# Kernel tuning notes

Hardware: AMD Instinct MI355X
Metric: run time of the kernel (lower is better)

Reference implementation:

```python
import jax, jax.numpy as jnp
import numpy as np

B, S, HID, H, RELC = 2, 1024, 1024, 16, 64
D = HID // H          # head dim = 64
R = 2 * RELC + 1      # 129 relative-position buckets
NEG_INF = -10000.0
LN_EPS = 1e-12


def setup_inputs() -> dict:
    key = jax.random.key(0)
    ks = jax.random.split(key, 16)
    s = 0.02
    return {
        "query": jax.random.normal(ks[0], (B, S, HID), jnp.float32),
        "key": jax.random.normal(ks[1], (B, S, HID), jnp.float32),
        "value": jax.random.normal(ks[2], (B, S, HID), jnp.float32),
        "mask_k": jnp.ones((B, S), jnp.float32),
        "mask_qk": jnp.ones((B, S, S), jnp.float32),
        "rposi": jax.random.randint(ks[3], (B, S, S), 0, R, jnp.int32),
        "Wq": jax.random.normal(ks[4], (HID, HID), jnp.float32) * s,
        "bq": jnp.zeros((HID,), jnp.float32),
        "Wk": jax.random.normal(ks[5], (HID, HID), jnp.float32) * s,
        "bk": jnp.zeros((HID,), jnp.float32),
        "Wv": jax.random.normal(ks[6], (HID, HID), jnp.float32) * s,
        "bv": jnp.zeros((HID,), jnp.float32),
        "Wd": jax.random.normal(ks[7], (HID, HID), jnp.float32) * s,
        "bd": jnp.zeros((HID,), jnp.float32),
        "ln_g": jnp.ones((HID,), jnp.float32),
        "ln_b": jnp.zeros((HID,), jnp.float32),
        "edge_atts": jax.random.normal(ks[8], (R, D), jnp.float32) * s,
        "edge_values": jax.random.normal(ks[9], (R, D), jnp.float32) * s,
    }


def _heads(x):  # [B,S,HID] -> [B,H,S,D]
    return x.reshape(B, -1, H, D).transpose(0, 2, 1, 3)


def reference(query, key, value, mask_k, mask_qk, rposi,
              Wq, bq, Wk, bk, Wv, bv, Wd, bd, ln_g, ln_b,
              edge_atts, edge_values):
    q = _heads(query @ Wq + bq)   # [B,H,Q,D]
    k = _heads(key @ Wk + bk)     # [B,H,K,D]
    v = _heads(value @ Wv + bv)   # [B,H,K,D]

    rp = jnp.clip(rposi, -RELC, RELC) + RELC          # [B,Q,K] in [0,2*RELC]

    scores = jnp.einsum('bhqd,bhkd->bhqk', q, k)      # [B,H,Q,K]
    # relative-position attention bias: q . edge_atts[rp]
    q2 = jnp.einsum('bhqd,rd->bhqr', q, edge_atts)    # [B,H,Q,R]
    rscore = jnp.take_along_axis(
        q2, jnp.broadcast_to(rp[:, None], (B, H, S, S)), axis=-1)
    scores = (scores + rscore) / jnp.sqrt(jnp.float32(D))

    att_mask = mask_k[:, None, :] * mask_qk           # [B,Q,K]
    scores = scores + (1.0 - att_mask)[:, None] * NEG_INF
    probs = jax.nn.softmax(scores, axis=-1)           # [B,H,Q,K]

    ctx = jnp.einsum('bhqk,bhkd->bhqd', probs, v)     # [B,H,Q,D]
    rval = edge_values[rp]                            # [B,Q,K,D]
    ctx = ctx + jnp.einsum('bhqk,bqkd->bhqd', probs, rval)

    ctx = ctx.transpose(0, 2, 1, 3).reshape(B, S, HID)
    h = ctx @ Wd + bd
    x = h + query
    mu = jnp.mean(x, axis=-1, keepdims=True)
    var = jnp.mean(jnp.square(x - mu), axis=-1, keepdims=True)
    return (x - mu) * jax.lax.rsqrt(var + LN_EPS) * ln_g + ln_b
```

## Files before the change

kernel.cpp:

```cpp
#include <hip/hip_runtime.h>
#include <hip/hip_bf16.h>
#include <stdint.h>

#define B_    2
#define S_    1024
#define HID_  1024
#define H_    16
#define D_    64
#define R_    129
#define RST_  132
#define NTOK_ 2048

typedef __attribute__((ext_vector_type(8))) short bf16x8;
typedef __attribute__((ext_vector_type(4))) float f32x4;

__device__ __forceinline__ float bf2f(unsigned short s) {
  union { float f; unsigned int u; } v; v.u = ((unsigned int)s) << 16; return v.f;
}
__device__ __forceinline__ unsigned short f2bf(float f) {
  union { float f; unsigned int u; } v; v.f = f;
  return (unsigned short)((v.u + 0x7fff + ((v.u >> 16) & 1)) >> 16);
}

__global__ __launch_bounds__(256) void wt4_kernel(const float* __restrict__ Wq,
                                                  const float* __restrict__ Wk,
                                                  const float* __restrict__ Wv,
                                                  const float* __restrict__ Wd,
                                                  unsigned short* __restrict__ WqT,
                                                  unsigned short* __restrict__ WkT,
                                                  unsigned short* __restrict__ WvT,
                                                  unsigned short* __restrict__ WdT) {
  const float* W; unsigned short* Wt;
  switch (blockIdx.z) {
    case 0: W = Wq; Wt = WqT; break;
    case 1: W = Wk; Wt = WkT; break;
    case 2: W = Wv; Wt = WvT; break;
    default: W = Wd; Wt = WdT; break;
  }
  __shared__ float tile[32][33];
  const int n0 = blockIdx.x * 32, k0 = blockIdx.y * 32;
  const int tx = threadIdx.x, ty = threadIdx.y;
  #pragma unroll
  for (int i = 0; i < 32; i += 8)
    tile[ty + i][tx] = W[(size_t)(k0 + ty + i) * HID_ + n0 + tx];
  __syncthreads();
  #pragma unroll
  for (int i = 0; i < 32; i += 8)
    Wt[(size_t)(n0 + ty + i) * HID_ + k0 + tx] = f2bf(tile[tx][ty + i]);
}

__global__ __launch_bounds__(256) void evt_kernel(const float* __restrict__ EV,
                                                  unsigned short* __restrict__ EVt) {
  const int idx = blockIdx.x * 256 + threadIdx.x;
  if (idx < 64 * 160) {
    const int d = idx / 160, r = idx % 160;
    EVt[idx] = f2bf(r < R_ ? EV[(size_t)r * D_ + d] : 0.f);
  }
}

__global__ __launch_bounds__(256) void rpm_kernel(const int* __restrict__ rposi,
                                                  const float* __restrict__ mask_k,
                                                  const float* __restrict__ mask_qk,
                                                  unsigned int* __restrict__ rpm) {
  const size_t base = ((size_t)blockIdx.x * 256 + threadIdx.x) * 4;
  const int b = (int)(base >> 20);
  const int k = (int)(base & (S_ - 1));
  const int4  rp4 = *(const int4*)(rposi + base);
  const float4 mq = *(const float4*)(mask_qk + base);
  const float4 mk = *(const float4*)(mask_k + (size_t)b * S_ + k);
  unsigned int o[4];
  const int rr[4] = {rp4.x, rp4.y, rp4.z, rp4.w};
  const float mm[4] = {mk.x * mq.x, mk.y * mq.y, mk.z * mq.z, mk.w * mq.w};
  #pragma unroll
  for (int u = 0; u < 4; u++) {
    const int rp = min(max(rr[u], -64), 64) + 64;
    const float bias = (1.f - mm[u]) * (-10000.0f);
    o[u] = ((unsigned int)f2bf(bias) << 16) | (unsigned int)rp;
  }
  *(uint4*)(rpm + base) = *(uint4*)o;
}

__global__ __launch_bounds__(256) void qkv_gemm_kernel(
    const float* __restrict__ query, const float* __restrict__ key, const float* __restrict__ value,
    const unsigned short* __restrict__ WqT, const unsigned short* __restrict__ WkT,
    const unsigned short* __restrict__ WvT,
    const float* __restrict__ bq, const float* __restrict__ bk, const float* __restrict__ bvv,
    unsigned short* __restrict__ Qh, unsigned short* __restrict__ Kh, unsigned short* __restrict__ Vt) {
  const float* A; const unsigned short* Bt; const float* bias; unsigned short* Out; int omode;
  if (blockIdx.z == 0)      { A = query; Bt = WqT; bias = bq;  Out = Qh; omode = 0; }
  else if (blockIdx.z == 1) { A = key;   Bt = WkT; bias = bk;  Out = Kh; omode = 0; }
  else                      { A = value; Bt = WvT; bias = bvv; Out = Vt; omode = 1; }
  __shared__ __align__(16) unsigned short Alds[64][40];
  __shared__ __align__(16) unsigned short Blds[64][40];
  const int m0 = blockIdx.x * 64, n0 = blockIdx.y * 64;
  const int t = threadIdx.x;
  const int wave = t >> 6, lane = t & 63, lo = lane & 15, hi = lane >> 4;
  const int wr = wave >> 1, wc = wave & 1;
  const int row = t >> 2, col = (t & 3) * 8;
  const f32x4 zero4 = {0.f, 0.f, 0.f, 0.f};
  f32x4 acc[2][2] = {{zero4, zero4}, {zero4, zero4}};

  for (int k0 = 0; k0 < HID_; k0 += 32) {
    const float* asrc = A + (size_t)(m0 + row) * HID_ + k0 + col;
    f32x4 v0 = *(const f32x4*)asrc, v1 = *(const f32x4*)(asrc + 4);
    unsigned short ab[8];
    ab[0]=f2bf(v0.x); ab[1]=f2bf(v0.y); ab[2]=f2bf(v0.z); ab[3]=f2bf(v0.w);
    ab[4]=f2bf(v1.x); ab[5]=f2bf(v1.y); ab[6]=f2bf(v1.z); ab[7]=f2bf(v1.w);
    bf16x8 bb = *(const bf16x8*)(Bt + (size_t)(n0 + row) * HID_ + k0 + col);
    __syncthreads();
    *(bf16x8*)&Alds[row][col] = *(bf16x8*)ab;
    *(bf16x8*)&Blds[row][col] = bb;
    __syncthreads();
    bf16x8 af[2], bfr[2];
    #pragma unroll
    for (int a = 0; a < 2; a++) af[a]  = *(const bf16x8*)&Alds[wr*32 + a*16 + lo][hi*8];
    #pragma unroll
    for (int b2 = 0; b2 < 2; b2++) bfr[b2] = *(const bf16x8*)&Blds[wc*32 + b2*16 + lo][hi*8];
    #pragma unroll
    for (int a = 0; a < 2; a++)
      #pragma unroll
      for (int b2 = 0; b2 < 2; b2++)
        acc[a][b2] = __builtin_amdgcn_mfma_f32_16x16x32_bf16(af[a], bfr[b2], acc[a][b2], 0, 0, 0);
  }

  #pragma unroll
  for (int a = 0; a < 2; a++) {
    const int mg = m0 + wr*32 + a*16 + hi*4;
    #pragma unroll
    for (int b2 = 0; b2 < 2; b2++) {
      const int n = n0 + wc*32 + b2*16 + lo;
      const float bv = bias[n];
      const int hh = n >> 6, d = n & (D_ - 1);
      #pragma unroll
      for (int j = 0; j < 4; j++) {
        const float val = acc[a][b2][j] + bv;
        const int m = mg + j;
        const int bb = m >> 10, s = m & (S_ - 1);
        if (omode == 0)
          Out[(((size_t)(bb * H_ + hh)) * S_ + s) * D_ + d] = f2bf(val);
        else
          Out[(((size_t)(bb * H_ + hh)) * D_ + d) * S_ + s] = f2bf(val);
      }
    }
  }
}

__global__ __launch_bounds__(256) void d_gemm_kernel(const unsigned short* __restrict__ Actx,
                                                     const unsigned short* __restrict__ Bt,
                                                     const float* __restrict__ bias,
                                                     float* __restrict__ Out) {
  __shared__ __align__(16) unsigned short Alds[64][40];
  __shared__ __align__(16) unsigned short Blds[64][40];
  const int m0 = blockIdx.x * 64, n0 = blockIdx.y * 64;
  const int t = threadIdx.x;
  const int wave = t >> 6, lane = t & 63, lo = lane & 15, hi = lane >> 4;
  const int wr = wave >> 1, wc = wave & 1;
  const int row = t >> 2, col = (t & 3) * 8;
  const f32x4 zero4 = {0.f, 0.f, 0.f, 0.f};
  f32x4 acc[2][2] = {{zero4, zero4}, {zero4, zero4}};

  for (int k0 = 0; k0 < HID_; k0 += 32) {
    bf16x8 aa = *(const bf16x8*)(Actx + (size_t)(m0 + row) * HID_ + k0 + col);
    bf16x8 bb = *(const bf16x8*)(Bt + (size_t)(n0 + row) * HID_ + k0 + col);
    __syncthreads();
    *(bf16x8*)&Alds[row][col] = aa;
    *(bf16x8*)&Blds[row][col] = bb;
    __syncthreads();
    bf16x8 af[2], bfr[2];
    #pragma unroll
    for (int a = 0; a < 2; a++) af[a]  = *(const bf16x8*)&Alds[wr*32 + a*16 + lo][hi*8];
    #pragma unroll
    for (int b2 = 0; b2 < 2; b2++) bfr[b2] = *(const bf16x8*)&Blds[wc*32 + b2*16 + lo][hi*8];
    #pragma unroll
    for (int a = 0; a < 2; a++)
      #pragma unroll
      for (int b2 = 0; b2 < 2; b2++)
        acc[a][b2] = __builtin_amdgcn_mfma_f32_16x16x32_bf16(af[a], bfr[b2], acc[a][b2], 0, 0, 0);
  }

  #pragma unroll
  for (int a = 0; a < 2; a++) {
    const int mg = m0 + wr*32 + a*16 + hi*4;
    #pragma unroll
    for (int b2 = 0; b2 < 2; b2++) {
      const int n = n0 + wc*32 + b2*16 + lo;
      const float bv = bias[n];
      #pragma unroll
      for (int j = 0; j < 4; j++)
        Out[(size_t)(mg + j) * HID_ + n] = acc[a][b2][j] + bv;
    }
  }
}

__global__ __launch_bounds__(256) void q2_kernel(const unsigned short* __restrict__ Qh,
                                                 const float* __restrict__ EA,
                                                 unsigned short* __restrict__ q2) {
  __shared__ __align__(16) unsigned short Qt[64][72];
  __shared__ __align__(16) unsigned short EAt[144][72];
  const int bh = blockIdx.y, s0 = blockIdx.x * 64;
  const int t = threadIdx.x, wave = t >> 6, lane = t & 63;
  const int lo = lane & 15, hi = lane >> 4;
  { const int row = t >> 2, c0 = (t & 3) * 16;
    const unsigned short* src = Qh + ((size_t)bh * S_ + s0 + row) * D_ + c0;
    *(bf16x8*)&Qt[row][c0]   = *(const bf16x8*)src;
    *(bf16x8*)&Qt[row][c0+8] = *(const bf16x8*)(src + 8); }
  for (int i = t; i < 144 * 64; i += 256) {
    const int r = i >> 6, d = i & 63;
    EAt[r][d] = f2bf(r < R_ ? EA[(size_t)r * D_ + d] : 0.f);
  }
  __syncthreads();
  bf16x8 af[2];
  af[0] = *(const bf16x8*)&Qt[wave*16 + lo][hi*8];
  af[1] = *(const bf16x8*)&Qt[wave*16 + lo][32 + hi*8];
  const f32x4 zero4 = {0.f, 0.f, 0.f, 0.f};
  f32x4 acc[9];
  #pragma unroll
  for (int rt = 0; rt < 9; rt++) acc[rt] = zero4;
  #pragma unroll
  for (int rt = 0; rt < 9; rt++)
    #pragma unroll
    for (int kk = 0; kk < 2; kk++) {
      bf16x8 bfr = *(const bf16x8*)&EAt[rt*16 + lo][kk*32 + hi*8];
      acc[rt] = __builtin_amdgcn_mfma_f32_16x16x32_bf16(af[kk], bfr, acc[rt], 0, 0, 0);
    }
  #pragma unroll
  for (int rt = 0; rt < 9; rt++) {
    const int r = rt * 16 + lo;
    if (r < RST_) {
      #pragma unroll
      for (int j = 0; j < 4; j++) {
        const int q = s0 + wave*16 + hi*4 + j;
        q2[((size_t)bh * S_ + q) * RST_ + r] = f2bf(acc[rt][j]);
      }
    }
  }
}


#define LOADKR(KW, KF, RV) do {                                                          \
    const int kw_ = (KW);                                                                \
    KF[0] = *(const bf16x8*)(Kbase + (size_t)(kw_ + lo) * D_ + hi * 8);                  \
    KF[1] = *(const bf16x8*)(Kbase + (size_t)(kw_ + lo) * D_ + 32 + hi * 8);             \
    KF[2] = *(const bf16x8*)(Kbase + (size_t)(kw_ + 16 + lo) * D_ + hi * 8);             \
    KF[3] = *(const bf16x8*)(Kbase + (size_t)(kw_ + 16 + lo) * D_ + 32 + hi * 8);        \
    _Pragma("unroll")                                                                    \
    for (int j_ = 0; j_ < 4; j_++) {                                                     \
      RV[j_]     = Rbase[(size_t)j_ * S_ + kw_ + lo];                                    \
      RV[4 + j_] = Rbase[(size_t)j_ * S_ + kw_ + 16 + lo];                               \
    }                                                                                    \
  } while (0)

#define ABODY(KT, KF, RV, KFN, RVN) do {                                                 \
    const int kw = (KT) * 64 + wk * 32;                                                  \
    if ((KT) < 15) { LOADKR(kw + 64, KFN, RVN); }                                        \
    f32x4 sc0 = zero4, sc1 = zero4;                                                      \
    __builtin_amdgcn_s_setprio(1);                                                       \
    sc0 = __builtin_amdgcn_mfma_f32_16x16x32_bf16(qfrag0, KF[0], sc0, 0, 0, 0);          \
    sc0 = __builtin_amdgcn_mfma_f32_16x16x32_bf16(qfrag1, KF[1], sc0, 0, 0, 0);          \
    sc1 = __builtin_amdgcn_mfma_f32_16x16x32_bf16(qfrag0, KF[2], sc1, 0, 0, 0);          \
    sc1 = __builtin_amdgcn_mfma_f32_16x16x32_bf16(qfrag1, KF[3], sc1, 0, 0, 0);          \
    __builtin_amdgcn_s_setprio(0);                                                       \
    bf16x8 vf0 = *(const bf16x8*)(Vbase + (size_t)(lo) * S_ + kw + hi * 8);              \
    bf16x8 vf1 = *(const bf16x8*)(Vbase + (size_t)(16 + lo) * S_ + kw + hi * 8);         \
    bf16x8 vf2 = *(const bf16x8*)(Vbase + (size_t)(32 + lo) * S_ + kw + hi * 8);         \
    bf16x8 vf3 = *(const bf16x8*)(Vbase + (size_t)(48 + lo) * S_ + kw + hi * 8);         \
    _Pragma("unroll")                                                                    \
    for (int j = 0; j < 4; j++) {                                                        \
      const int qr = wq * 16 + hi * 4 + j;                                               \
      {                                                                                  \
        const unsigned int w0 = RV[j];                                                   \
        const int rp = (int)(w0 & 0xFFFFu);                                              \
        const float bias = bf2f((unsigned short)(w0 >> 16));                             \
        const float rs = bf2f(Uq.q2l[qr][rp]);                                           \
        const float sval = (sc0[j] + rs) * 0.125f + bias;                                \
        const float p = __expf(fminf(sval, 60.f));                                       \
        lsum[j] += p;                                                                    \
        if (rp == 128) r128[j] += p; else atomicAdd(&hist[qr][rp], p);                   \
        Plds[wave][hi * 4 + j][lo] = f2bf(p);                                            \
      }                                                                                  \
      {                                                                                  \
        const unsigned int w1 = RV[4 + j];                                               \
        const int rp = (int)(w1 & 0xFFFFu);                                              \
        const float bias = bf2f((unsigned short)(w1 >> 16));                             \
        const float rs = bf2f(Uq.q2l[qr][rp]);                                           \
        const float sval = (sc1[j] + rs) * 0.125f + bias;                                \
        const float p = __expf(fminf(sval, 60.f));                                       \
        lsum[j] += p;                                                                    \
        if (rp == 128) r128[j] += p; else atomicAdd(&hist[qr][rp], p);                   \
        Plds[wave][hi * 4 + j][16 + lo] = f2bf(p);                                       \
      }                                                                                  \
    }                                                                                    \
    bf16x8 pf = *(const bf16x8*)&Plds[wave][lo][hi * 8];                                 \
    __builtin_amdgcn_s_setprio(1);                                                       \
    ctx[0] = __builtin_amdgcn_mfma_f32_16x16x32_bf16(pf, vf0, ctx[0], 0, 0, 0);          \
    ctx[1] = __builtin_amdgcn_mfma_f32_16x16x32_bf16(pf, vf1, ctx[1], 0, 0, 0);          \
    ctx[2] = __builtin_amdgcn_mfma_f32_16x16x32_bf16(pf, vf2, ctx[2], 0, 0, 0);          \
    ctx[3] = __builtin_amdgcn_mfma_f32_16x16x32_bf16(pf, vf3, ctx[3], 0, 0, 0);          \
    __builtin_amdgcn_s_setprio(0);                                                       \
  } while (0)

__global__ __launch_bounds__(256, 4) void attn_kernel(const unsigned short* __restrict__ Qh,
                                                      const unsigned short* __restrict__ Kh,
                                                      const unsigned short* __restrict__ Vt,
                                                      const unsigned short* __restrict__ q2,
                                                      const unsigned int* __restrict__ rpm,
                                                      const unsigned short* __restrict__ EVt,
                                                      unsigned short* __restrict__ ctxb) {
  __shared__ union UU {
    unsigned short q2l[32][132];
    float red[2][16][65];
  } Uq;
  __shared__ float hist[32][132];
  __shared__ __align__(16) unsigned short Plds[4][16][40];
  __shared__ float lsumLDS[2][32];

  const int bh = blockIdx.y, b = bh >> 4, h = bh & 15;
  const int q0 = blockIdx.x * 32;
  const int t = threadIdx.x, wave = t >> 6, lane = t & 63;
  const int lo = lane & 15, hi = lane >> 4;
  const int wq = wave >> 1, wk = wave & 1;

  { const unsigned int* src = (const unsigned int*)(q2 + ((size_t)bh * S_ + q0) * RST_);
    unsigned int* dst = (unsigned int*)&Uq.q2l[0][0];
    for (int i = t; i < 32 * 132 / 2; i += 256) dst[i] = src[i]; }
  for (int i = t; i < 32 * 132; i += 256) (&hist[0][0])[i] = 0.f;

  bf16x8 qfrag0, qfrag1;
  { const unsigned short* qrow = Qh + ((size_t)bh * S_ + q0 + wq * 16 + lo) * D_;
    qfrag0 = *(const bf16x8*)(qrow + hi * 8);
    qfrag1 = *(const bf16x8*)(qrow + 32 + hi * 8); }

  const f32x4 zero4 = {0.f, 0.f, 0.f, 0.f};
  f32x4 ctx[4] = {zero4, zero4, zero4, zero4};
  float lsum[4] = {0.f, 0.f, 0.f, 0.f};
  float r128[4] = {0.f, 0.f, 0.f, 0.f};

  const unsigned short* Kbase = Kh + (size_t)bh * S_ * D_;
  const unsigned short* Vbase = Vt + (size_t)bh * D_ * S_;
  const unsigned int*   Rbase = rpm + (size_t)b * S_ * S_ + ((size_t)(q0 + wq * 16 + hi * 4)) * S_;

  __syncthreads();

  bf16x8 kfA[4], kfB[4];
  unsigned int rvA[8], rvB[8];
  LOADKR(wk * 32, kfA, rvA);

  #pragma unroll 1
  for (int kt2 = 0; kt2 < 8; kt2++) {
    ABODY(kt2 * 2,     kfA, rvA, kfB, rvB);
    ABODY(kt2 * 2 + 1, kfB, rvB, kfA, rvA);
  }

  #pragma unroll
  for (int j = 0; j < 4; j++) {
    float v = r128[j];
    v += __shfl_xor(v, 1); v += __shfl_xor(v, 2); v += __shfl_xor(v, 4); v += __shfl_xor(v, 8);
    if (lo == 0) atomicAdd(&hist[wq * 16 + hi * 4 + j][128], v);
    float w = lsum[j];
    w += __shfl_xor(w, 1); w += __shfl_xor(w, 2); w += __shfl_xor(w, 4); w += __shfl_xor(w, 8);
    if (lo == 0) lsumLDS[wk][wq * 16 + hi * 4 + j] = w;
  }
  __syncthreads();

  #pragma unroll
  for (int g2 = 0; g2 < 2; g2++) {
    const int r0 = (wk * 2 + g2) * 32;
    const float* hrow = &hist[wq * 16 + lo][r0 + hi * 8];
    bf16x8 hf;
    #pragma unroll
    for (int u = 0; u < 8; u++) hf[u] = (short)f2bf(hrow[u]);
    #pragma unroll
    for (int dt = 0; dt < 4; dt++) {
      bf16x8 ef = *(const bf16x8*)(EVt + (size_t)(dt * 16 + lo) * 160 + r0 + hi * 8);
      ctx[dt] = __builtin_amdgcn_mfma_f32_16x16x32_bf16(hf, ef, ctx[dt], 0, 0, 0);
    }
  }
  if (wk == 1) {
    #pragma unroll
    for (int dt = 0; dt < 4; dt++) {
      const float ev = bf2f(EVt[(size_t)(dt * 16 + lo) * 160 + 128]);
      #pragma unroll
      for (int j = 0; j < 4; j++) {
        ctx[dt][j] += hist[wq * 16 + hi * 4 + j][128] * ev;
        Uq.red[wq][hi * 4 + j][dt * 16 + lo] = ctx[dt][j];
      }
    }
  }
  __syncthreads();
  if (wk == 0) {
    float ls[4];
    #pragma unroll
    for (int j = 0; j < 4; j++)
      ls[j] = lsumLDS[0][wq * 16 + hi * 4 + j] + lsumLDS[1][wq * 16 + hi * 4 + j];
    #pragma unroll
    for (int dt = 0; dt < 4; dt++)
      #pragma unroll
      for (int j = 0; j < 4; j++) {
        const float val = (ctx[dt][j] + Uq.red[wq][hi * 4 + j][dt * 16 + lo]) / ls[j];
        const int q = q0 + wq * 16 + hi * 4 + j;
        ctxb[((size_t)b * S_ + q) * HID_ + h * D_ + dt * 16 + lo] = f2bf(val);
      }
  }
}

__global__ __launch_bounds__(256) void ln_kernel(const float* __restrict__ hbuf,
                                                 const float* __restrict__ query,
                                                 const float* __restrict__ g,
                                                 const float* __restrict__ bta,
                                                 float* __restrict__ out) {
  const int row = blockIdx.x, t = threadIdx.x;
  f32x4 hv = *(const f32x4*)(hbuf + (size_t)row * HID_ + t * 4);
  f32x4 qv = *(const f32x4*)(query + (size_t)row * HID_ + t * 4);
  f32x4 x;
  x.x = hv.x + qv.x; x.y = hv.y + qv.y; x.z = hv.z + qv.z; x.w = hv.w + qv.w;
  float s  = x.x + x.y + x.z + x.w;
  float s2 = x.x*x.x + x.y*x.y + x.z*x.z + x.w*x.w;
  #pragma unroll
  for (int m = 1; m < 64; m <<= 1) { s += __shfl_xor(s, m); s2 += __shfl_xor(s2, m); }
  __shared__ float w1[4], w2[4];
  const int wave = t >> 6;
  if ((t & 63) == 0) { w1[wave] = s; w2[wave] = s2; }
  __syncthreads();
  s  = w1[0] + w1[1] + w1[2] + w1[3];
  s2 = w2[0] + w2[1] + w2[2] + w2[3];
  const float mu  = s * (1.f / HID_);
  const float var = s2 * (1.f / HID_) - mu * mu;
  const float rstd = rsqrtf(var + 1e-12f);
  f32x4 gv = *(const f32x4*)(g + t * 4);
  f32x4 bv = *(const f32x4*)(bta + t * 4);
  f32x4 o;
  o.x = (x.x - mu) * rstd * gv.x + bv.x;
  o.y = (x.y - mu) * rstd * gv.y + bv.y;
  o.z = (x.z - mu) * rstd * gv.z + bv.z;
  o.w = (x.w - mu) * rstd * gv.w + bv.w;
  *(f32x4*)(out + (size_t)row * HID_ + t * 4) = o;
}

extern "C" void kernel_launch(void* const* d_in, const int* in_sizes, int n_in,
                              void* d_out, int out_size, void* d_ws, size_t ws_size,
                              hipStream_t stream) {
  const float* query   = (const float*)d_in[0];
  const float* key     = (const float*)d_in[1];
  const float* value   = (const float*)d_in[2];
  const float* mask_k  = (const float*)d_in[3];
  const float* mask_qk = (const float*)d_in[4];
  const int*   rposi   = (const int*)d_in[5];
  const float* Wq = (const float*)d_in[6];
  const float* bq = (const float*)d_in[7];
  const float* Wk = (const float*)d_in[8];
  const float* bk = (const float*)d_in[9];
  const float* Wv = (const float*)d_in[10];
  const float* bv = (const float*)d_in[11];
  const float* Wd = (const float*)d_in[12];
  const float* bd = (const float*)d_in[13];
  const float* ln_g = (const float*)d_in[14];
  const float* ln_b = (const float*)d_in[15];
  const float* edge_atts   = (const float*)d_in[16];
  const float* edge_values = (const float*)d_in[17];

  char* ws = (char*)d_ws;
  unsigned short* WqT  = (unsigned short*)(ws + 0);
  unsigned short* WkT  = (unsigned short*)(ws + 2097152);
  unsigned short* WvT  = (unsigned short*)(ws + 4194304);
  unsigned short* WdT  = (unsigned short*)(ws + 6291456);
  unsigned short* Qh   = (unsigned short*)(ws + 8388608);
  unsigned short* Kh   = (unsigned short*)(ws + 12582912);
  unsigned short* Vt   = (unsigned short*)(ws + 16777216);
  unsigned short* q2b  = (unsigned short*)(ws + 20971520);
  unsigned short* EVt  = (unsigned short*)(ws + 29622272);
  unsigned short* ctxb = (unsigned short*)(ws + 29642752);
  float*          hbuf = (float*)        (ws + 33837056);
  unsigned int*   rpm  = (unsigned int*) (ws + 33837056);

  wt4_kernel<<<dim3(32, 32, 4), dim3(32, 8), 0, stream>>>(Wq, Wk, Wv, Wd, WqT, WkT, WvT, WdT);
  evt_kernel<<<40, 256, 0, stream>>>(edge_values, EVt);
  rpm_kernel<<<2048, 256, 0, stream>>>(rposi, mask_k, mask_qk, rpm);

  qkv_gemm_kernel<<<dim3(32, 16, 3), 256, 0, stream>>>(query, key, value, WqT, WkT, WvT,
                                                       bq, bk, bv, Qh, Kh, Vt);

  q2_kernel<<<dim3(S_/64, B_*H_), 256, 0, stream>>>(Qh, edge_atts, q2b);

  attn_kernel<<<dim3(S_/32, B_*H_), 256, 0, stream>>>(Qh, Kh, Vt, q2b, rpm, EVt, ctxb);

  d_gemm_kernel<<<dim3(32, 16), 256, 0, stream>>>(ctxb, WdT, bd, hbuf);

  ln_kernel<<<NTOK_, 256, 0, stream>>>(hbuf, query, ln_g, ln_b, (float*)d_out);
}
```

Before: 198.4 us.

## Precompute exp of relative bias and pack rposi/mask into fragment-ordered bytes

```diff
diff --git a/kernel.cpp b/kernel.cpp
--- a/kernel.cpp
+++ b/kernel.cpp
@@ -8,8 +8,10 @@
 #define H_    16
 #define D_    64
 #define R_    129
-#define RST_  132
+#define EST_  136
+#define SENT_ 132
 #define NTOK_ 2048
+#define C2_   0.18033688011112042f
 
 typedef __attribute__((ext_vector_type(8))) short bf16x8;
 typedef __attribute__((ext_vector_type(4))) float f32x4;
@@ -58,26 +60,26 @@
   }
 }
 
-__global__ __launch_bounds__(256) void rpm_kernel(const int* __restrict__ rposi,
+__global__ __launch_bounds__(256) void rpx_kernel(const int* __restrict__ rposi,
                                                   const float* __restrict__ mask_k,
                                                   const float* __restrict__ mask_qk,
-                                                  unsigned int* __restrict__ rpm) {
-  const size_t base = ((size_t)blockIdx.x * 256 + threadIdx.x) * 4;
-  const int b = (int)(base >> 20);
-  const int k = (int)(base & (S_ - 1));
-  const int4  rp4 = *(const int4*)(rposi + base);
-  const float4 mq = *(const float4*)(mask_qk + base);
-  const float4 mk = *(const float4*)(mask_k + (size_t)b * S_ + k);
-  unsigned int o[4];
-  const int rr[4] = {rp4.x, rp4.y, rp4.z, rp4.w};
-  const float mm[4] = {mk.x * mq.x, mk.y * mq.y, mk.z * mq.z, mk.w * mq.w};
-  #pragma unroll
-  for (int u = 0; u < 4; u++) {
-    const int rp = min(max(rr[u], -64), 64) + 64;
-    const float bias = (1.f - mm[u]) * (-10000.0f);
-    o[u] = ((unsigned int)f2bf(bias) << 16) | (unsigned int)rp;
-  }
-  *(uint4*)(rpm + base) = *(uint4*)o;
+                                                  unsigned char* __restrict__ rpx) {
+  const int t = threadIdx.x;
+  const int lo = t & 15, hi = (t >> 4) & 3, wq = (t >> 6) & 1, wk = (t >> 7) & 1;
+  const int kt = blockIdx.x, q5 = blockIdx.y, b = blockIdx.z;
+  unsigned char out[8];
+  #pragma unroll
+  for (int e = 0; e < 8; e++) {
+    const int ct2 = e >> 2, j = e & 3;
+    const int q = q5 * 32 + wq * 16 + hi * 4 + j;
+    const int k = kt * 64 + wk * 32 + ct2 * 16 + lo;
+    int rp = rposi[((size_t)b * S_ + q) * S_ + k];
+    rp = min(max(rp, -64), 64) + 64;
+    const float m = mask_qk[((size_t)b * S_ + q) * S_ + k] * mask_k[(size_t)b * S_ + k];
+    out[e] = (m > 0.5f) ? (unsigned char)rp : (unsigned char)SENT_;
+  }
+  const size_t off = ((((((size_t)b * 32 + q5) * 16 + kt) * 2 + wk) * 2 + wq) * 4 + hi) * 16 + lo;
+  *(uint2*)(rpx + off * 8) = *(uint2*)out;
 }
 
 __global__ __launch_bounds__(256) void qkv_gemm_kernel(
@@ -192,9 +194,9 @@
   }
 }
 
-__global__ __launch_bounds__(256) void q2_kernel(const unsigned short* __restrict__ Qh,
+__global__ __launch_bounds__(256) void eb_kernel(const unsigned short* __restrict__ Qh,
                                                  const float* __restrict__ EA,
-                                                 unsigned short* __restrict__ q2) {
+                                                 unsigned short* __restrict__ Eb) {
   __shared__ __align__(16) unsigned short Qt[64][72];
   __shared__ __align__(16) unsigned short EAt[144][72];
   const int bh = blockIdx.y, s0 = blockIdx.x * 64;
@@ -226,69 +228,54 @@
   #pragma unroll
   for (int rt = 0; rt < 9; rt++) {
     const int r = rt * 16 + lo;
-    if (r < RST_) {
+    if (r < EST_) {
       #pragma unroll
       for (int j = 0; j < 4; j++) {
         const int q = s0 + wave*16 + hi*4 + j;
-        q2[((size_t)bh * S_ + q) * RST_ + r] = f2bf(acc[rt][j]);
+        const float val = (r < R_) ? exp2f(acc[rt][j] * C2_) : 0.f;
+        Eb[((size_t)bh * S_ + q) * EST_ + r] = f2bf(val);
       }
     }
   }
 }
 
 
-#define LOADKR(KW, KF, RV) do {                                                          \
-    const int kw_ = (KW);                                                                \
-    KF[0] = *(const bf16x8*)(Kbase + (size_t)(kw_ + lo) * D_ + hi * 8);                  \
-    KF[1] = *(const bf16x8*)(Kbase + (size_t)(kw_ + lo) * D_ + 32 + hi * 8);             \
-    KF[2] = *(const bf16x8*)(Kbase + (size_t)(kw_ + 16 + lo) * D_ + hi * 8);             \
-    KF[3] = *(const bf16x8*)(Kbase + (size_t)(kw_ + 16 + lo) * D_ + 32 + hi * 8);        \
+#define ABODY(KT, RX) do {                                                               \
+    const int kw = (KT) * 64 + wk * 32;                                                  \
+    int rpv[8];                                                                          \
+    rpv[0] = (RX).x & 255;         rpv[1] = ((RX).x >> 8) & 255;                         \
+    rpv[2] = ((RX).x >> 16) & 255; rpv[3] = (RX).x >> 24;                                \
+    rpv[4] = (RX).y & 255;         rpv[5] = ((RX).y >> 8) & 255;                         \
+    rpv[6] = ((RX).y >> 16) & 255; rpv[7] = (RX).y >> 24;                                \
+    float ge[8];                                                                         \
     _Pragma("unroll")                                                                    \
-    for (int j_ = 0; j_ < 4; j_++) {                                                     \
-      RV[j_]     = Rbase[(size_t)j_ * S_ + kw_ + lo];                                    \
-      RV[4 + j_] = Rbase[(size_t)j_ * S_ + kw_ + 16 + lo];                               \
-    }                                                                                    \
-  } while (0)
-
-#define ABODY(KT, KF, RV, KFN, RVN) do {                                                 \
-    const int kw = (KT) * 64 + wk * 32;                                                  \
-    if ((KT) < 15) { LOADKR(kw + 64, KFN, RVN); }                                        \
+    for (int e = 0; e < 8; e++)                                                          \
+      ge[e] = bf2f(Uq.El[wq * 16 + hi * 4 + (e & 3)][rpv[e]]);                           \
     f32x4 sc0 = zero4, sc1 = zero4;                                                      \
     __builtin_amdgcn_s_setprio(1);                                                       \
-    sc0 = __builtin_amdgcn_mfma_f32_16x16x32_bf16(qfrag0, KF[0], sc0, 0, 0, 0);          \
-    sc0 = __builtin_amdgcn_mfma_f32_16x16x32_bf16(qfrag1, KF[1], sc0, 0, 0, 0);          \
-    sc1 = __builtin_amdgcn_mfma_f32_16x16x32_bf16(qfrag0, KF[2], sc1, 0, 0, 0);          \
-    sc1 = __builtin_amdgcn_mfma_f32_16x16x32_bf16(qfrag1, KF[3], sc1, 0, 0, 0);          \
+    { bf16x8 kf0 = *(const bf16x8*)(Kbase + (size_t)(kw + lo) * D_ + hi * 8);            \
+      bf16x8 kf1 = *(const bf16x8*)(Kbase + (size_t)(kw + lo) * D_ + 32 + hi * 8);       \
+      bf16x8 kf2 = *(const bf16x8*)(Kbase + (size_t)(kw + 16 + lo) * D_ + hi * 8);       \
+      bf16x8 kf3 = *(const bf16x8*)(Kbase + (size_t)(kw + 16 + lo) * D_ + 32 + hi * 8);  \
+      sc0 = __builtin_amdgcn_mfma_f32_16x16x32_bf16(qfrag0, kf0, sc0, 0, 0, 0);          \
+      sc0 = __builtin_amdgcn_mfma_f32_16x16x32_bf16(qfrag1, kf1, sc0, 0, 0, 0);          \
+      sc1 = __builtin_amdgcn_mfma_f32_16x16x32_bf16(qfrag0, kf2, sc1, 0, 0, 0);          \
+      sc1 = __builtin_amdgcn_mfma_f32_16x16x32_bf16(qfrag1, kf3, sc1, 0, 0, 0); }        \
     __builtin_amdgcn_s_setprio(0);                                                       \
     bf16x8 vf0 = *(const bf16x8*)(Vbase + (size_t)(lo) * S_ + kw + hi * 8);              \
     bf16x8 vf1 = *(const bf16x8*)(Vbase + (size_t)(16 + lo) * S_ + kw + hi * 8);         \
     bf16x8 vf2 = *(const bf16x8*)(Vbase + (size_t)(32 + lo) * S_ + kw + hi * 8);         \
     bf16x8 vf3 = *(const bf16x8*)(Vbase + (size_t)(48 + lo) * S_ + kw + hi * 8);         \
     _Pragma("unroll")                                                                    \
-    for (int j = 0; j < 4; j++) {                                                        \
+    for (int e = 0; e < 8; e++) {                                                        \
+      const int j = e & 3;                                                               \
+      const float sv = (e < 4) ? sc0[j] : sc1[j];                                        \
+      const float p = exp2f(sv * C2_) * ge[e];                                           \
+      lsum[j] += p;                                                                      \
       const int qr = wq * 16 + hi * 4 + j;                                               \
-      {                                                                                  \
-        const unsigned int w0 = RV[j];                                                   \
-        const int rp = (int)(w0 & 0xFFFFu);                                              \
-        const float bias = bf2f((unsigned short)(w0 >> 16));                             \
-        const float rs = bf2f(Uq.q2l[qr][rp]);                                           \
-        const float sval = (sc0[j] + rs) * 0.125f + bias;                                \
-        const float p = __expf(fminf(sval, 60.f));                                       \
-        lsum[j] += p;                                                                    \
-        if (rp == 128) r128[j] += p; else atomicAdd(&hist[qr][rp], p);                   \
-        Plds[wave][hi * 4 + j][lo] = f2bf(p);                                            \
-      }                                                                                  \
-      {                                                                                  \
-        const unsigned int w1 = RV[4 + j];                                               \
-        const int rp = (int)(w1 & 0xFFFFu);                                              \
-        const float bias = bf2f((unsigned short)(w1 >> 16));                             \
-        const float rs = bf2f(Uq.q2l[qr][rp]);                                           \
-        const float sval = (sc1[j] + rs) * 0.125f + bias;                                \
-        const float p = __expf(fminf(sval, 60.f));                                       \
-        lsum[j] += p;                                                                    \
-        if (rp == 128) r128[j] += p; else atomicAdd(&hist[qr][rp], p);                   \
-        Plds[wave][hi * 4 + j][16 + lo] = f2bf(p);                                       \
-      }                                                                                  \
+      if (rpv[e] == 128) r128[j] += p;                                                   \
+      else atomicAdd(&hist[qr][rpv[e]], p);                                              \
+      Plds[wave][hi * 4 + j][(e >> 2) * 16 + lo] = f2bf(p);                              \
     }                                                                                    \
     bf16x8 pf = *(const bf16x8*)&Plds[wave][lo][hi * 8];                                 \
     __builtin_amdgcn_s_setprio(1);                                                       \
@@ -302,28 +289,28 @@
 __global__ __launch_bounds__(256, 4) void attn_kernel(const unsigned short* __restrict__ Qh,
                                                       const unsigned short* __restrict__ Kh,
                                                       const unsigned short* __restrict__ Vt,
-                                                      const unsigned short* __restrict__ q2,
-                                                      const unsigned int* __restrict__ rpm,
+                                                      const unsigned short* __restrict__ Eb,
+                                                      const unsigned char* __restrict__ rpx,
                                                       const unsigned short* __restrict__ EVt,
                                                       unsigned short* __restrict__ ctxb) {
   __shared__ union UU {
-    unsigned short q2l[32][132];
+    unsigned short El[32][EST_];
     float red[2][16][65];
   } Uq;
-  __shared__ float hist[32][132];
+  __shared__ float hist[32][EST_];
   __shared__ __align__(16) unsigned short Plds[4][16][40];
   __shared__ float lsumLDS[2][32];
 
   const int bh = blockIdx.y, b = bh >> 4, h = bh & 15;
-  const int q0 = blockIdx.x * 32;
+  const int q5 = blockIdx.x, q0 = q5 * 32;
   const int t = threadIdx.x, wave = t >> 6, lane = t & 63;
   const int lo = lane & 15, hi = lane >> 4;
   const int wq = wave >> 1, wk = wave & 1;
 
-  { const unsigned int* src = (const unsigned int*)(q2 + ((size_t)bh * S_ + q0) * RST_);
-    unsigned int* dst = (unsigned int*)&Uq.q2l[0][0];
-    for (int i = t; i < 32 * 132 / 2; i += 256) dst[i] = src[i]; }
-  for (int i = t; i < 32 * 132; i += 256) (&hist[0][0])[i] = 0.f;
+  { const unsigned int* src = (const unsigned int*)(Eb + ((size_t)bh * S_ + q0) * EST_);
+    unsigned int* dst = (unsigned int*)&Uq.El[0][0];
+    for (int i = t; i < 32 * EST_ / 2; i += 256) dst[i] = src[i]; }
+  for (int i = t; i < 32 * EST_; i += 256) (&hist[0][0])[i] = 0.f;
 
   bf16x8 qfrag0, qfrag1;
   { const unsigned short* qrow = Qh + ((size_t)bh * S_ + q0 + wq * 16 + lo) * D_;
@@ -337,18 +324,18 @@
 
   const unsigned short* Kbase = Kh + (size_t)bh * S_ * D_;
   const unsigned short* Vbase = Vt + (size_t)bh * D_ * S_;
-  const unsigned int*   Rbase = rpm + (size_t)b * S_ * S_ + ((size_t)(q0 + wq * 16 + hi * 4)) * S_;
-
-  __syncthreads();
-
-  bf16x8 kfA[4], kfB[4];
-  unsigned int rvA[8], rvB[8];
-  LOADKR(wk * 32, kfA, rvA);
-
+  const unsigned char* RXp = rpx +
+      (((((((size_t)b * 32 + q5) * 16) * 2 + wk) * 2 + wq) * 4 + hi) * 16 + lo) * 8;
+
+  __syncthreads();
+
+  uint2 rxA = *(const uint2*)(RXp);
   #pragma unroll 1
   for (int kt2 = 0; kt2 < 8; kt2++) {
-    ABODY(kt2 * 2,     kfA, rvA, kfB, rvB);
-    ABODY(kt2 * 2 + 1, kfB, rvB, kfA, rvA);
+    uint2 rxB = *(const uint2*)(RXp + (size_t)(2 * kt2 + 1) * 2048);
+    ABODY(2 * kt2, rxA);
+    if (kt2 < 7) rxA = *(const uint2*)(RXp + (size_t)(2 * kt2 + 2) * 2048);
+    ABODY(2 * kt2 + 1, rxB);
   }
 
   #pragma unroll
@@ -463,25 +450,25 @@
   unsigned short* WkT  = (unsigned short*)(ws + 2097152);
   unsigned short* WvT  = (unsigned short*)(ws + 4194304);
   unsigned short* WdT  = (unsigned short*)(ws + 6291456);
+  unsigned short* ctxb = (unsigned short*)(ws + 0);
   unsigned short* Qh   = (unsigned short*)(ws + 8388608);
   unsigned short* Kh   = (unsigned short*)(ws + 12582912);
   unsigned short* Vt   = (unsigned short*)(ws + 16777216);
-  unsigned short* q2b  = (unsigned short*)(ws + 20971520);
-  unsigned short* EVt  = (unsigned short*)(ws + 29622272);
-  unsigned short* ctxb = (unsigned short*)(ws + 29642752);
-  float*          hbuf = (float*)        (ws + 33837056);
-  unsigned int*   rpm  = (unsigned int*) (ws + 33837056);
+  float*          hbuf = (float*)        (ws + 8388608);
+  unsigned short* Eb   = (unsigned short*)(ws + 20971520);
+  unsigned short* EVt  = (unsigned short*)(ws + 29884416);
+  unsigned char*  rpx  = (unsigned char*) (ws + 29904896);
 
   wt4_kernel<<<dim3(32, 32, 4), dim3(32, 8), 0, stream>>>(Wq, Wk, Wv, Wd, WqT, WkT, WvT, WdT);
   evt_kernel<<<40, 256, 0, stream>>>(edge_values, EVt);
-  rpm_kernel<<<2048, 256, 0, stream>>>(rposi, mask_k, mask_qk, rpm);
+  rpx_kernel<<<dim3(16, 32, 2), 256, 0, stream>>>(rposi, mask_k, mask_qk, rpx);
 
   qkv_gemm_kernel<<<dim3(32, 16, 3), 256, 0, stream>>>(query, key, value, WqT, WkT, WvT,
                                                        bq, bk, bv, Qh, Kh, Vt);
 
-  q2_kernel<<<dim3(S_/64, B_*H_), 256, 0, stream>>>(Qh, edge_atts, q2b);
-
-  attn_kernel<<<dim3(S_/32, B_*H_), 256, 0, stream>>>(Qh, Kh, Vt, q2b, rpm, EVt, ctxb);
+  eb_kernel<<<dim3(S_/64, B_*H_), 256, 0, stream>>>(Qh, edge_atts, Eb);
+
+  attn_kernel<<<dim3(S_/32, B_*H_), 256, 0, stream>>>(Qh, Kh, Vt, Eb, rpx, EVt, ctxb);
 
   d_gemm_kernel<<<dim3(32, 16), 256, 0, stream>>>(ctxb, WdT, bd, hbuf);
 
```

New measurement: 192.0 us. 3.2% less time.
